# Kernel optimization log

Measured on AMD Instinct MI355X. Metric: run time of the kernel, lower is better.

The kernel has to match this reference:

```python
import math
import jax, jax.numpy as jnp
import numpy as np

N_HEADS = 16

def setup_inputs() -> dict:
    key = jax.random.key(0)
    k1, k2, k3 = jax.random.split(key, 3)
    B, T, C = 2, 2048, 1024
    x = jax.random.normal(k1, (B, T, C), dtype=jnp.float32)
    # Linear weights stored as [in, out] so y = x @ W + b (same math as torch Linear)
    w_qkv = jax.random.normal(k2, (C, 3 * C), dtype=jnp.float32) * (1.0 / math.sqrt(C))
    b_qkv = jnp.zeros((3 * C,), dtype=jnp.float32)
    w_out = jax.random.normal(k3, (C, C), dtype=jnp.float32) * (1.0 / math.sqrt(C))
    b_out = jnp.zeros((C,), dtype=jnp.float32)
    return {"x": x, "w_qkv": w_qkv, "b_qkv": b_qkv, "w_out": w_out, "b_out": b_out}

def reference(x, w_qkv, b_qkv, w_out, b_out):
    B, T, C = x.shape
    H = N_HEADS
    hd = C // H
    qkv = (x @ w_qkv + b_qkv).reshape(B, T, 3, H, hd)
    q, k, v = qkv[:, :, 0], qkv[:, :, 1], qkv[:, :, 2]  # [B,T,H,hd]
    scale = 1.0 / math.sqrt(hd)
    att = jnp.einsum('bqhd,bkhd->bhqk', q, k) * scale  # [B,H,T,T]
    causal = jnp.tril(jnp.ones((T, T), dtype=bool))
    att = jnp.where(causal[None, None], att, jnp.float32(-jnp.inf))
    att = jax.nn.softmax(att, axis=-1)
    # dropout p=0.0 -> identity (eval mode)
    y = jnp.einsum('bhqk,bkhd->bqhd', att, v).reshape(B, T, C)
    return y @ w_out + b_out
```

## Files before the change

### kernel.cpp

```cpp
#include <hip/hip_runtime.h>
#include <hip/hip_bf16.h>
#include <stdint.h>


typedef __bf16 bf16_t;
typedef __attribute__((ext_vector_type(8))) __bf16 bf16x8;
typedef __attribute__((ext_vector_type(4))) __bf16 bf16x4;
typedef __attribute__((ext_vector_type(4))) short short4v;
typedef __attribute__((ext_vector_type(4))) float f32x4;

static_assert(sizeof(bf16x8) == 16, "bf16x8 must be 16B");

#if defined(__has_builtin)
#if __has_builtin(__builtin_amdgcn_mfma_f32_16x16x16bf16_1k)
#define HAVE_MFMA16 1
#endif
#if __has_builtin(__builtin_amdgcn_exp2f)
#define EXP2F(x) __builtin_amdgcn_exp2f(x)
#endif
#endif
#ifndef HAVE_MFMA16
#define HAVE_MFMA16 0
#endif
#ifndef EXP2F
#define EXP2F(x) exp2f(x)
#endif

__device__ inline void async_copy16(const bf16_t* gsrc, bf16_t* lds_dst) {
  __builtin_amdgcn_global_load_lds(
      (const __attribute__((address_space(1))) uint32_t*)(const void*)gsrc,
      (__attribute__((address_space(3))) uint32_t*)(void*)lds_dst,
      16, 0, 0);
}

__global__ __launch_bounds__(256) void prep_kernel(
    const float* __restrict__ x, const float* __restrict__ wq,
    const float* __restrict__ wo, bf16_t* __restrict__ xb,
    bf16_t* __restrict__ wqkvT, bf16_t* __restrict__ woutT) {
  __shared__ bf16_t tile[32][33];
  const int bid = blockIdx.x;
  if (bid < 2048) {
    const int i = bid * 256 + threadIdx.x;
    const float4* s = (const float4*)x;
    float4 a = s[i * 2], b = s[i * 2 + 1];
    bf16x8 o;
    o[0] = (bf16_t)a.x; o[1] = (bf16_t)a.y; o[2] = (bf16_t)a.z; o[3] = (bf16_t)a.w;
    o[4] = (bf16_t)b.x; o[5] = (bf16_t)b.y; o[6] = (bf16_t)b.z; o[7] = (bf16_t)b.w;
    ((bf16x8*)xb)[i] = o;
    return;
  }
  const bool isq = bid < 5120;
  const int id = isq ? bid - 2048 : bid - 5120;
  const int C = isq ? 3072 : 1024;
  const int R = 1024;
  const int nbx = isq ? 96 : 32;
  const float* in = isq ? wq : wo;
  bf16_t* out = isq ? wqkvT : woutT;
  const int c0 = (id % nbx) * 32, r0 = (id / nbx) * 32;
  const int tx = threadIdx.x & 31;
  const int ty = threadIdx.x >> 5;
#pragma unroll
  for (int i = 0; i < 4; i++) {
    int r = ty + i * 8;
    tile[r][tx] = (bf16_t)in[(size_t)(r0 + r) * C + c0 + tx];
  }
  __syncthreads();
#pragma unroll
  for (int i = 0; i < 4; i++) {
    int r = ty + i * 8;
    out[(size_t)(c0 + r) * R + r0 + tx] = tile[tx][r];
  }
}

template <bool OUT_F32>
__global__ __launch_bounds__(256) void gemm_bt_kernel(
    const bf16_t* __restrict__ A, const bf16_t* __restrict__ Bt,
    const float* __restrict__ bias, void* __restrict__ Cv, int M, int N,
    int K) {
  __shared__ __align__(16) bf16_t sA[128 * 32];
  __shared__ __align__(16) bf16_t sB[128 * 32];
  const int tid = threadIdx.x;
  const int wave = tid >> 6, lane = tid & 63;
  const int quad = lane >> 4, l16 = lane & 15;
  const int wm = (wave >> 1) * 64, wn = (wave & 1) * 64;
  const int bm = blockIdx.y * 128, bn = blockIdx.x * 128;

  const int srow = wave * 16 + (lane >> 2);
  const int skk = (lane & 3) * 8;
  const bf16_t* gA = A + (size_t)(bm + srow) * K + skk;
  const bf16_t* gB = Bt + (size_t)(bn + srow) * K + skk;
  bf16_t* lA = sA + wave * 512;
  bf16_t* lB = sB + wave * 512;

  f32x4 acc[4][4] = {};

  for (int k0 = 0; k0 < K; k0 += 32) {
    __syncthreads();
    async_copy16(gA + k0, lA);
    async_copy16(gA + (size_t)64 * K + k0, lA + 2048);
    async_copy16(gB + k0, lB);
    async_copy16(gB + (size_t)64 * K + k0, lB + 2048);
    __syncthreads();

    bf16x8 af[4], bfr[4];
#pragma unroll
    for (int i = 0; i < 4; i++)
      af[i] = *(const bf16x8*)&sA[(wm + i * 16 + l16) * 32 + quad * 8];
#pragma unroll
    for (int j = 0; j < 4; j++)
      bfr[j] = *(const bf16x8*)&sB[(wn + j * 16 + l16) * 32 + quad * 8];
#pragma unroll
    for (int i = 0; i < 4; i++)
#pragma unroll
      for (int j = 0; j < 4; j++)
        acc[i][j] = __builtin_amdgcn_mfma_f32_16x16x32_bf16(af[i], bfr[j],
                                                            acc[i][j], 0, 0, 0);
  }

#pragma unroll
  for (int j = 0; j < 4; j++) {
    const int col = bn + wn + j * 16 + l16;
    const float bv = bias[col];
#pragma unroll
    for (int i = 0; i < 4; i++) {
#pragma unroll
      for (int r = 0; r < 4; r++) {
        const int row = bm + wm + i * 16 + quad * 4 + r;
        const float v = acc[i][j][r] + bv;
        if (OUT_F32)
          ((float*)Cv)[(size_t)row * N + col] = v;
        else
          ((bf16_t*)Cv)[(size_t)row * N + col] = (bf16_t)v;
      }
    }
  }
}

__global__ __launch_bounds__(256) void gemm_bt64_kernel(
    const bf16_t* __restrict__ A, const bf16_t* __restrict__ Bt,
    const float* __restrict__ bias, float* __restrict__ C, int M, int N,
    int K) {
  __shared__ __align__(16) bf16_t sA[64 * 32];
  __shared__ __align__(16) bf16_t sB[128 * 32];
  const int tid = threadIdx.x;
  const int wave = tid >> 6, lane = tid & 63;
  const int quad = lane >> 4, l16 = lane & 15;
  const int wm = (wave >> 1) * 32, wn = (wave & 1) * 64;
  const int bm = blockIdx.y * 64, bn = blockIdx.x * 128;

  const int srow = wave * 16 + (lane >> 2);
  const int skk = (lane & 3) * 8;
  const bf16_t* gA = A + (size_t)(bm + srow) * K + skk;
  const bf16_t* gB = Bt + (size_t)(bn + srow) * K + skk;
  bf16_t* lA = sA + wave * 512;
  bf16_t* lB = sB + wave * 512;

  f32x4 acc[2][4] = {};

  for (int k0 = 0; k0 < K; k0 += 32) {
    __syncthreads();
    async_copy16(gA + k0, lA);
    async_copy16(gB + k0, lB);
    async_copy16(gB + (size_t)64 * K + k0, lB + 2048);
    __syncthreads();

    bf16x8 af[2], bfr[4];
#pragma unroll
    for (int i = 0; i < 2; i++)
      af[i] = *(const bf16x8*)&sA[(wm + i * 16 + l16) * 32 + quad * 8];
#pragma unroll
    for (int j = 0; j < 4; j++)
      bfr[j] = *(const bf16x8*)&sB[(wn + j * 16 + l16) * 32 + quad * 8];
#pragma unroll
    for (int i = 0; i < 2; i++)
#pragma unroll
      for (int j = 0; j < 4; j++)
        acc[i][j] = __builtin_amdgcn_mfma_f32_16x16x32_bf16(af[i], bfr[j],
                                                            acc[i][j], 0, 0, 0);
  }

#pragma unroll
  for (int j = 0; j < 4; j++) {
    const int col = bn + wn + j * 16 + l16;
    const float bv = bias[col];
#pragma unroll
    for (int i = 0; i < 2; i++) {
#pragma unroll
      for (int r = 0; r < 4; r++) {
        const int row = bm + wm + i * 16 + quad * 4 + r;
        C[(size_t)row * N + col] = acc[i][j][r] + bv;
      }
    }
  }
}

#if HAVE_MFMA16
__global__ __launch_bounds__(256, 4) void attn_kernel(
    const bf16_t* __restrict__ qkv, bf16_t* __restrict__ Y) {
  constexpr int T = 2048, C3 = 3072;
  constexpr float CSC = 0.18033688f;
  constexpr float MB = 20.0f;
  __shared__ __align__(16) bf16_t sK[2][64 * 64];
  __shared__ __align__(16) bf16_t sVt[2][64 * 64];

  const int tid = threadIdx.x;
  const int wave = tid >> 6, lane = tid & 63;
  const int quad = lane >> 4, l16 = lane & 15;
  const int bh = blockIdx.y;
  const int flip = (bh >> 3) & 1;
  const int vv = ((int)blockIdx.x + ((bh >> 4) & 1) * 8) & 31;
  const int X = flip ? (31 - vv) : vv;
  const int q0 = X * 64;
  const int b = bh >> 4, h = bh & 15;
  const size_t base = (size_t)b * T * C3 + (size_t)h * 64;

  const int qrow = q0 + wave * 16 + l16;
  const bf16x8 qf0 = *(const bf16x8*)&qkv[base + (size_t)qrow * C3 + quad * 8];
  const bf16x8 qf1 =
      *(const bf16x8*)&qkv[base + (size_t)qrow * C3 + 32 + quad * 8];

  f32x4 o[4] = {};
  f32x4 l4 = {0.f, 0.f, 0.f, 0.f};

  const int t = tid >> 2, seg = tid & 3;
  const bf16_t* gK = &qkv[base + (size_t)t * C3 + 1024 + seg * 16];
  const int kq = tid >> 4, dq = tid & 15;
  const bf16_t* gV = &qkv[base + (size_t)(4 * kq) * C3 + 2048 + dq * 4];

  bf16x8 kr0 = *(const bf16x8*)gK;
  bf16x8 kr1 = *(const bf16x8*)(gK + 8);
  bf16x4 vA0 = *(const bf16x4*)gV;
  bf16x4 vA1 = *(const bf16x4*)(gV + C3);
  bf16x4 vA2 = *(const bf16x4*)(gV + 2 * C3);
  bf16x4 vA3 = *(const bf16x4*)(gV + 3 * C3);

  for (int kt = 0; kt < X; kt++) {
    const int p = kt & 1;
    *(bf16x8*)&sK[p][t * 64 + (((2 * seg + 0) ^ (t & 7)) << 3)] = kr0;
    *(bf16x8*)&sK[p][t * 64 + (((2 * seg + 1) ^ (t & 7)) << 3)] = kr1;
#pragma unroll
    for (int i = 0; i < 4; i++) {
      const int d = dq * 4 + i;
      bf16x4 w;
      w[0] = vA0[i]; w[1] = vA1[i]; w[2] = vA2[i]; w[3] = vA3[i];
      *(bf16x4*)&sVt[p][d * 64 + ((kq ^ (d & 15)) << 2)] = w;
    }
    {
      const size_t off = (size_t)(kt + 1) * 64 * C3;
      kr0 = *(const bf16x8*)(gK + off);
      kr1 = *(const bf16x8*)(gK + off + 8);
      vA0 = *(const bf16x4*)(gV + off);
      vA1 = *(const bf16x4*)(gV + off + C3);
      vA2 = *(const bf16x4*)(gV + off + 2 * C3);
      vA3 = *(const bf16x4*)(gV + off + 3 * C3);
    }
    __syncthreads();

#pragma unroll
    for (int j = 0; j < 4; j++) {
      const int trow = j * 16 + l16;
      bf16x8 kf0 =
          *(const bf16x8*)&sK[p][trow * 64 + ((quad ^ (trow & 7)) << 3)];
      bf16x8 kf1 =
          *(const bf16x8*)&sK[p][trow * 64 + (((4 + quad) ^ (trow & 7)) << 3)];
      f32x4 s2 = {};
      __builtin_amdgcn_s_setprio(1);
      s2 = __builtin_amdgcn_mfma_f32_16x16x32_bf16(kf0, qf0, s2, 0, 0, 0);
      s2 = __builtin_amdgcn_mfma_f32_16x16x32_bf16(kf1, qf1, s2, 0, 0, 0);
      __builtin_amdgcn_s_setprio(0);
#pragma unroll
      for (int r = 0; r < 4; r++) s2[r] = EXP2F(fmaf(s2[r], CSC, -MB));
      l4 += s2;
      bf16x4 pb;
      pb[0] = (bf16_t)s2[0]; pb[1] = (bf16_t)s2[1];
      pb[2] = (bf16_t)s2[2]; pb[3] = (bf16_t)s2[3];
      union { bf16x4 bv; short4v sv; } u;
      u.bv = pb;
      const short4v pa = u.sv;
      __builtin_amdgcn_s_setprio(1);
#pragma unroll
      for (int n16 = 0; n16 < 4; n16++) {
        const int d = n16 * 16 + l16;
        const short4v vf = *(const short4v*)&sVt[p][d * 64 +
                                                    (((j * 4 + quad) ^ (d & 15))
                                                     << 2)];
        o[n16] =
            __builtin_amdgcn_mfma_f32_16x16x16bf16_1k(pa, vf, o[n16], 0, 0, 0);
      }
      __builtin_amdgcn_s_setprio(0);
    }
  }

  {
    const int p = X & 1;
    *(bf16x8*)&sK[p][t * 64 + (((2 * seg + 0) ^ (t & 7)) << 3)] = kr0;
    *(bf16x8*)&sK[p][t * 64 + (((2 * seg + 1) ^ (t & 7)) << 3)] = kr1;
#pragma unroll
    for (int i = 0; i < 4; i++) {
      const int d = dq * 4 + i;
      bf16x4 w;
      w[0] = vA0[i]; w[1] = vA1[i]; w[2] = vA2[i]; w[3] = vA3[i];
      *(bf16x4*)&sVt[p][d * 64 + ((kq ^ (d & 15)) << 2)] = w;
    }
    __syncthreads();

#pragma unroll
    for (int j = 0; j < 4; j++) {
      if (j > wave) continue;
      const int trow = j * 16 + l16;
      bf16x8 kf0 =
          *(const bf16x8*)&sK[p][trow * 64 + ((quad ^ (trow & 7)) << 3)];
      bf16x8 kf1 =
          *(const bf16x8*)&sK[p][trow * 64 + (((4 + quad) ^ (trow & 7)) << 3)];
      f32x4 s2 = {};
      __builtin_amdgcn_s_setprio(1);
      s2 = __builtin_amdgcn_mfma_f32_16x16x32_bf16(kf0, qf0, s2, 0, 0, 0);
      s2 = __builtin_amdgcn_mfma_f32_16x16x32_bf16(kf1, qf1, s2, 0, 0, 0);
      __builtin_amdgcn_s_setprio(0);
      const bool diag = (j == wave);
#pragma unroll
      for (int r = 0; r < 4; r++) {
        float pv = EXP2F(fmaf(s2[r], CSC, -MB));
        if (diag && (quad * 4 + r > l16)) pv = 0.f;
        s2[r] = pv;
      }
      l4 += s2;
      bf16x4 pb;
      pb[0] = (bf16_t)s2[0]; pb[1] = (bf16_t)s2[1];
      pb[2] = (bf16_t)s2[2]; pb[3] = (bf16_t)s2[3];
      union { bf16x4 bv; short4v sv; } u;
      u.bv = pb;
      const short4v pa = u.sv;
      __builtin_amdgcn_s_setprio(1);
#pragma unroll
      for (int n16 = 0; n16 < 4; n16++) {
        const int d = n16 * 16 + l16;
        const short4v vf = *(const short4v*)&sVt[p][d * 64 +
                                                    (((j * 4 + quad) ^ (d & 15))
                                                     << 2)];
        o[n16] =
            __builtin_amdgcn_mfma_f32_16x16x16bf16_1k(pa, vf, o[n16], 0, 0, 0);
      }
      __builtin_amdgcn_s_setprio(0);
    }
  }

  float l_acc = (l4[0] + l4[1]) + (l4[2] + l4[3]);
  l_acc += __shfl_xor(l_acc, 16);
  l_acc += __shfl_xor(l_acc, 32);
#pragma unroll
  for (int r = 0; r < 4; r++) {
    const float lr = __shfl(l_acc, quad * 4 + r);
    const float inv = 1.0f / lr;
    const int row = q0 + wave * 16 + quad * 4 + r;
#pragma unroll
    for (int n16 = 0; n16 < 4; n16++)
      Y[((size_t)b * T + row) * 1024 + h * 64 + n16 * 16 + l16] =
          (bf16_t)(o[n16][r] * inv);
  }
}
#else
__global__ __launch_bounds__(256, 4) void attn_kernel(
    const bf16_t* __restrict__ qkv, bf16_t* __restrict__ Y) {
  constexpr int T = 2048, C3 = 3072;
  constexpr float CSC = 0.18033688f;
  constexpr float MB = 20.0f;
  __shared__ __align__(16) bf16_t sK[64 * 64];
  __shared__ __align__(16) bf16_t sVt[64 * 64];
  __shared__ __align__(16) bf16_t sP[4][16 * 64];

  const int tid = threadIdx.x;
  const int wave = tid >> 6, lane = tid & 63;
  const int quad = lane >> 4, l16 = lane & 15;
  const int bh = blockIdx.y;
  const int flip = (bh >> 3) & 1;
  const int vv = ((int)blockIdx.x + ((bh >> 4) & 1) * 8) & 31;
  const int X = flip ? (31 - vv) : vv;
  const int q0 = X * 64;
  const int b = bh >> 4, h = bh & 15;
  const size_t base = (size_t)b * T * C3 + (size_t)h * 64;

  const int qrow = q0 + wave * 16 + l16;
  const bf16x8 qf0 = *(const bf16x8*)&qkv[base + (size_t)qrow * C3 + quad * 8];
  const bf16x8 qf1 =
      *(const bf16x8*)&qkv[base + (size_t)qrow * C3 + 32 + quad * 8];

  f32x4 o[4] = {};
  float l_i[4] = {0.f, 0.f, 0.f, 0.f};

  const int t = tid >> 2, seg = tid & 3;
  const int tk = t & 7, tg3 = t >> 3;
  const bf16_t* gK = &qkv[base + (size_t)t * C3 + 1024 + seg * 16];
  const bf16_t* gV = &qkv[base + (size_t)t * C3 + 2048 + seg * 16];

  const int ktiles = X + 1;

  bf16x8 kr0 = *(const bf16x8*)gK;
  bf16x8 kr1 = *(const bf16x8*)(gK + 8);
  bf16x8 vr0 = *(const bf16x8*)gV;
  bf16x8 vr1 = *(const bf16x8*)(gV + 8);

  for (int kt = 0; kt < ktiles; kt++) {
    __syncthreads();
    *(bf16x8*)&sK[t * 64 + (((2 * seg + 0) ^ tk) << 3)] = kr0;
    *(bf16x8*)&sK[t * 64 + (((2 * seg + 1) ^ tk) << 3)] = kr1;
#pragma unroll
    for (int i = 0; i < 8; i++) {
      const int d = seg * 16 + i;
      sVt[d * 64 + ((tg3 ^ (d >> 3)) << 3) + (t & 7)] = vr0[i];
    }
#pragma unroll
    for (int i = 0; i < 8; i++) {
      const int d = seg * 16 + 8 + i;
      sVt[d * 64 + ((tg3 ^ (d >> 3)) << 3) + (t & 7)] = vr1[i];
    }
    __syncthreads();

    if (kt + 1 < ktiles) {
      const size_t off = (size_t)(kt + 1) * 64 * C3;
      kr0 = *(const bf16x8*)(gK + off);
      kr1 = *(const bf16x8*)(gK + off + 8);
      vr0 = *(const bf16x8*)(gV + off);
      vr1 = *(const bf16x8*)(gV + off + 8);
    }

    f32x4 s[4] = {};
#pragma unroll
    for (int j = 0; j < 4; j++) {
      const int kkey = l16 & 7;
      bf16x8 kf0 =
          *(const bf16x8*)&sK[(j * 16 + l16) * 64 + ((quad ^ kkey) << 3)];
      bf16x8 kf1 =
          *(const bf16x8*)&sK[(j * 16 + l16) * 64 + (((4 + quad) ^ kkey) << 3)];
      s[j] = __builtin_amdgcn_mfma_f32_16x16x32_bf16(qf0, kf0, s[j], 0, 0, 0);
      s[j] = __builtin_amdgcn_mfma_f32_16x16x32_bf16(qf1, kf1, s[j], 0, 0, 0);
    }

#pragma unroll
    for (int j = 0; j < 4; j++)
#pragma unroll
      for (int r = 0; r < 4; r++) s[j][r] = EXP2F(fmaf(s[j][r], CSC, -MB));
    if (kt == ktiles - 1) {
      const int k0 = kt * 64;
#pragma unroll
      for (int j = 0; j < 4; j++) {
        const int kcol = k0 + j * 16 + l16;
#pragma unroll
        for (int r = 0; r < 4; r++)
          if (kcol > q0 + wave * 16 + quad * 4 + r) s[j][r] = 0.f;
      }
    }
#pragma unroll
    for (int j = 0; j < 4; j++)
#pragma unroll
      for (int r = 0; r < 4; r++) l_i[r] += s[j][r];

    bf16_t* sp = &sP[wave][0];
#pragma unroll
    for (int j = 0; j < 4; j++)
#pragma unroll
      for (int r = 0; r < 4; r++) {
        const int m = quad * 4 + r;
        const int kw = (m + (m >> 3)) & 7;
        sp[m * 64 + ((((2 * j + (l16 >> 3)) ^ kw)) << 3) + (l16 & 7)] =
            (bf16_t)s[j][r];
      }

    const int kap = (l16 + (l16 >> 3)) & 7;
#pragma unroll
    for (int s2 = 0; s2 < 2; s2++) {
      bf16x8 pf =
          *(const bf16x8*)&sp[l16 * 64 + (((4 * s2 + quad) ^ kap) << 3)];
#pragma unroll
      for (int j = 0; j < 4; j++) {
        const int d = j * 16 + l16;
        bf16x8 vf =
            *(const bf16x8*)&sVt[d * 64 + (((4 * s2 + quad) ^ (d >> 3)) << 3)];
        o[j] = __builtin_amdgcn_mfma_f32_16x16x32_bf16(pf, vf, o[j], 0, 0, 0);
      }
    }
  }

#pragma unroll
  for (int r = 0; r < 4; r++) {
    float l = l_i[r];
#pragma unroll
    for (int off = 1; off < 16; off <<= 1) l += __shfl_xor(l, off);
    const float inv = 1.0f / l;
    const int row = q0 + wave * 16 + quad * 4 + r;
#pragma unroll
    for (int j = 0; j < 4; j++)
      Y[((size_t)b * T + row) * 1024 + h * 64 + j * 16 + l16] =
          (bf16_t)(o[j][r] * inv);
  }
}
#endif

extern "C" void kernel_launch(void* const* d_in, const int* in_sizes, int n_in,
                              void* d_out, int out_size, void* d_ws,
                              size_t ws_size, hipStream_t stream) {
  const float* x = nullptr;
  const float* w_qkv = nullptr;
  const float* b_qkv = nullptr;
  const float* w_out = nullptr;
  const float* b_out = nullptr;
  for (int i = 0; i < n_in; i++) {
    switch (in_sizes[i]) {
      case 4194304: x = (const float*)d_in[i]; break;
      case 3145728: w_qkv = (const float*)d_in[i]; break;
      case 3072:    b_qkv = (const float*)d_in[i]; break;
      case 1048576: w_out = (const float*)d_in[i]; break;
      case 1024:    b_out = (const float*)d_in[i]; break;
      default: break;
    }
  }
  float* out = (float*)d_out;

  bf16_t* xb = (bf16_t*)d_ws;
  bf16_t* wqkvT = xb + (size_t)4194304;
  bf16_t* woutT = wqkvT + (size_t)3145728;
  bf16_t* qkv = woutT + (size_t)1048576;
  bf16_t* Y = qkv + (size_t)12582912;

  prep_kernel<<<6144, 256, 0, stream>>>(x, w_qkv, w_out, xb, wqkvT, woutT);
  gemm_bt_kernel<false><<<dim3(24, 32), 256, 0, stream>>>(
      xb, wqkvT, b_qkv, (void*)qkv, 4096, 3072, 1024);
  attn_kernel<<<dim3(32, 32), 256, 0, stream>>>(qkv, Y);
  gemm_bt64_kernel<<<dim3(8, 64), 256, 0, stream>>>(
      Y, woutT, b_out, out, 4096, 1024, 1024);
}
```

Measured before the change: 185.7 us.

## Double GEMM K-tile to 64 with XOR-swizzled LDS layout

The bf16 GEMM kernel now stages 64-wide K slices per iteration instead of 32, which halves the number of barrier pairs and loop trips. Its LDS tile uses an XOR swizzle on 16-byte chunks so that MFMA operand reads avoid bank conflicts. The launch bounds ask for 3 blocks per CU. The kernel uses twice the shared memory per block, which may limit occupancy, and there is still no double buffering.

```diff
diff --git a/kernel.cpp b/kernel.cpp
--- a/kernel.cpp
+++ b/kernel.cpp
@@ -73,48 +73,60 @@
 }
 
 template <bool OUT_F32>
-__global__ __launch_bounds__(256) void gemm_bt_kernel(
+__global__ __launch_bounds__(256, 3) void gemm_bt_kernel(
     const bf16_t* __restrict__ A, const bf16_t* __restrict__ Bt,
     const float* __restrict__ bias, void* __restrict__ Cv, int M, int N,
     int K) {
-  __shared__ __align__(16) bf16_t sA[128 * 32];
-  __shared__ __align__(16) bf16_t sB[128 * 32];
+  __shared__ __align__(16) bf16_t sA[128 * 64];
+  __shared__ __align__(16) bf16_t sB[128 * 64];
   const int tid = threadIdx.x;
   const int wave = tid >> 6, lane = tid & 63;
   const int quad = lane >> 4, l16 = lane & 15;
   const int wm = (wave >> 1) * 64, wn = (wave & 1) * 64;
   const int bm = blockIdx.y * 128, bn = blockIdx.x * 128;
 
-  const int srow = wave * 16 + (lane >> 2);
-  const int skk = (lane & 3) * 8;
-  const bf16_t* gA = A + (size_t)(bm + srow) * K + skk;
-  const bf16_t* gB = Bt + (size_t)(bn + srow) * K + skk;
-  bf16_t* lA = sA + wave * 512;
-  bf16_t* lB = sB + wave * 512;
+  const int rl = lane >> 3, cl = lane & 7;
+  const int srow = wave * 32;
+  const bf16_t* gA =
+      A + (size_t)(bm + srow + rl) * K + (size_t)((cl ^ rl) << 3);
+  const bf16_t* gB =
+      Bt + (size_t)(bn + srow + rl) * K + (size_t)((cl ^ rl) << 3);
+  bf16_t* lA = sA + srow * 64;
+  bf16_t* lB = sB + srow * 64;
 
   f32x4 acc[4][4] = {};
 
-  for (int k0 = 0; k0 < K; k0 += 32) {
-    __syncthreads();
-    async_copy16(gA + k0, lA);
-    async_copy16(gA + (size_t)64 * K + k0, lA + 2048);
-    async_copy16(gB + k0, lB);
-    async_copy16(gB + (size_t)64 * K + k0, lB + 2048);
-    __syncthreads();
-
-    bf16x8 af[4], bfr[4];
-#pragma unroll
-    for (int i = 0; i < 4; i++)
-      af[i] = *(const bf16x8*)&sA[(wm + i * 16 + l16) * 32 + quad * 8];
-#pragma unroll
-    for (int j = 0; j < 4; j++)
-      bfr[j] = *(const bf16x8*)&sB[(wn + j * 16 + l16) * 32 + quad * 8];
-#pragma unroll
-    for (int i = 0; i < 4; i++)
-#pragma unroll
-      for (int j = 0; j < 4; j++)
-        acc[i][j] = __builtin_amdgcn_mfma_f32_16x16x32_bf16(af[i], bfr[j],
-                                                            acc[i][j], 0, 0, 0);
+  for (int k0 = 0; k0 < K; k0 += 64) {
+    __syncthreads();
+#pragma unroll
+    for (int c = 0; c < 4; c++) {
+      async_copy16(gA + (size_t)(c * 8) * K + k0, lA + c * 512);
+      async_copy16(gB + (size_t)(c * 8) * K + k0, lB + c * 512);
+    }
+    __syncthreads();
+
+#pragma unroll
+    for (int h = 0; h < 2; h++) {
+      bf16x8 af[4], bfr[4];
+#pragma unroll
+      for (int i = 0; i < 4; i++) {
+        const int row = wm + i * 16 + l16;
+        af[i] = *(const bf16x8*)&sA[row * 64 +
+                                    (((h * 4 + quad) ^ (row & 7)) << 3)];
+      }
+#pragma unroll
+      for (int j = 0; j < 4; j++) {
+        const int row = wn + j * 16 + l16;
+        bfr[j] = *(const bf16x8*)&sB[row * 64 +
+                                     (((h * 4 + quad) ^ (row & 7)) << 3)];
+      }
+#pragma unroll
+      for (int i = 0; i < 4; i++)
+#pragma unroll
+        for (int j = 0; j < 4; j++)
+          acc[i][j] = __builtin_amdgcn_mfma_f32_16x16x32_bf16(
+              af[i], bfr[j], acc[i][j], 0, 0, 0);
+    }
   }
 
 #pragma unroll
```

After: 178.6 us. 1.04x faster.
